# Kernel optimization log

Hardware: AMD Instinct MI355X
Metric: run time of the kernel (lower is better)

Reference implementation:

```python
import jax, jax.numpy as jnp
import numpy as np

T, E, K = 3, 6, 3            # n_tasks, num_experts, top-k
D, H, EH, TH = 1024, 1024, 1024, 1024  # input, hidden, expert hidden, tower hidden
B, C = 1024, 16              # batch, n_candidates


def setup_inputs() -> dict:
    key = jax.random.key(0)
    ks = jax.random.split(key, 16)
    s = 0.02
    return {
        "cls_embed": jax.random.normal(ks[0], (B, C, D), jnp.float32),
        "fc1_w": jax.random.normal(ks[1], (D, H), jnp.float32) * s,
        "fc1_b": jnp.zeros((H,), jnp.float32),
        "fc2_w": jax.random.normal(ks[2], (H, H), jnp.float32) * s,
        "fc2_b": jnp.zeros((H,), jnp.float32),
        "w_gate": jax.random.normal(ks[3], (T, H, E), jnp.float32) * s,
        "ew1": jax.random.normal(ks[4], (E, H, EH), jnp.float32) * s,
        "eb1": jnp.zeros((E, EH), jnp.float32),
        "ew2": jax.random.normal(ks[5], (E, EH, H), jnp.float32) * s,
        "eb2": jnp.zeros((E, H), jnp.float32),
        "tw1": jax.random.normal(ks[6], (T, H, TH), jnp.float32) * s,
        "tb1": jnp.zeros((T, TH), jnp.float32),
        "tw2": jax.random.normal(ks[7], (T, TH), jnp.float32) * s,
        "tb2": jnp.zeros((T,), jnp.float32),
    }


def reference(cls_embed, fc1_w, fc1_b, fc2_w, fc2_b, w_gate,
              ew1, eb1, ew2, eb2, tw1, tb1, tw2, tb2):
    # flatten (batch, candidate) -> N
    x = cls_embed.reshape(-1, cls_embed.shape[-1])            # [N, D]
    # shared bottom: fc2(relu(fc1(x)))
    h = jax.nn.relu(x @ fc1_w + fc1_b) @ fc2_w + fc2_b        # [N, H]
    # per-task top-k gating (clean/eval path of noisy top-k)
    logits = jnp.einsum('nh,the->tne', h, w_gate)             # [T, N, E]
    top_v, top_i = jax.lax.top_k(logits, K)                   # [T, N, K]
    top_w = jax.nn.softmax(top_v, axis=-1)                    # softmax over selected k
    onehot = jax.nn.one_hot(top_i, E, dtype=h.dtype)          # [T, N, K, E]
    gates = jnp.einsum('tnk,tnke->tne', top_w, onehot)        # sparse gate weights
    # experts: two-layer MLPs, computed densely then combined by sparse gates
    eh = jax.nn.relu(jnp.einsum('nh,ehm->nem', h, ew1) + eb1)  # [N, E, EH]
    eo = jnp.einsum('nem,emh->neh', eh, ew2) + eb2             # [N, E, H]
    mo = jnp.einsum('tne,neh->tnh', gates, eo)                 # [T, N, H]
    # per-task towers -> scalar logit per candidate
    th = jax.nn.relu(jnp.einsum('tnh,thm->tnm', mo, tw1) + tb1[:, None, :])
    out = jnp.einsum('tnm,tm->tn', th, tw2) + tb2[:, None]     # [T, N]
    return out
```

## Files before the change

kernel.cpp:

```cpp
#include <hip/hip_runtime.h>
#include <hip/hip_bf16.h>
#include <math.h>
#include <stdint.h>

#define NTOK 16384
#define DH   1024
#define NE   6
#define NT   3

typedef _Float16 f16x8 __attribute__((ext_vector_type(8)));
typedef float    f32x4 __attribute__((ext_vector_type(4)));

__device__ __forceinline__ void stage16(const _Float16* g, _Float16* lds_base, int lane)
{
#if __has_builtin(__builtin_amdgcn_global_load_lds)
    __builtin_amdgcn_global_load_lds(
        (const __attribute__((address_space(1))) unsigned int*)(uintptr_t)g,
        (__attribute__((address_space(3))) unsigned int*)(uintptr_t)lds_base, 16, 0, 0);
#else
    *(float4*)(lds_base + lane * 8) = *(const float4*)g;
#endif
}

__device__ __forceinline__ f32x4 mfma16(f16x8 a, f16x8 b, f32x4 c)
{
    return __builtin_amdgcn_mfma_f32_16x16x32_f16(a, b, c, 0, 0, 0);
}

__device__ __forceinline__ void mfma_tile(const _Float16* __restrict__ A,
                                          const _Float16* __restrict__ Bt,
                                          int n0, int m0, f32x4 acc[4][4])
{
    __shared__ __align__(16) _Float16 As[128 * 32];
    __shared__ __align__(16) _Float16 Bs[128 * 32];
    const int tid  = threadIdx.x;
    const int w    = tid >> 6, lane = tid & 63;
    const int lr   = lane >> 2;
    const int lk   = (lane & 3) * 8;
    const int wm   = (w >> 1) * 64, wn = (w & 1) * 64;
    const int fl   = lane & 15;
    const int fq   = (lane >> 4) * 8;

    const _Float16* ga0 = A  + (size_t)(n0 + w * 32 + lr) * DH + lk;
    const _Float16* ga1 = ga0 + 16 * DH;
    const _Float16* gb0 = Bt + (size_t)(m0 + w * 32 + lr) * DH + lk;
    const _Float16* gb1 = gb0 + 16 * DH;
    _Float16* la0 = As + (w * 32) * 32;
    _Float16* la1 = la0 + 16 * 32;
    _Float16* lb0 = Bs + (w * 32) * 32;
    _Float16* lb1 = lb0 + 16 * 32;

    for (int ks = 0; ks < DH; ks += 32) {
        __syncthreads();
        stage16(ga0 + ks, la0, lane);
        stage16(ga1 + ks, la1, lane);
        stage16(gb0 + ks, lb0, lane);
        stage16(gb1 + ks, lb1, lane);
        __syncthreads();
        f16x8 af[4], bf[4];
#pragma unroll
        for (int i = 0; i < 4; ++i)
            af[i] = *(const f16x8*)(As + (wm + i * 16 + fl) * 32 + fq);
#pragma unroll
        for (int j = 0; j < 4; ++j)
            bf[j] = *(const f16x8*)(Bs + (wn + j * 16 + fl) * 32 + fq);
#pragma unroll
        for (int i = 0; i < 4; ++i)
#pragma unroll
            for (int j = 0; j < 4; ++j)
                acc[i][j] = mfma16(af[i], bf[j], acc[i][j]);
    }
}

__device__ __forceinline__ void mfma_tile_split(const _Float16* __restrict__ Ah,
                                                const _Float16* __restrict__ Al,
                                                const _Float16* __restrict__ Bh,
                                                const _Float16* __restrict__ Bl,
                                                int n0, int m0, f32x4 acc[4][4])
{
    __shared__ __align__(16) _Float16 Ash[128 * 32];
    __shared__ __align__(16) _Float16 Asl[128 * 32];
    __shared__ __align__(16) _Float16 Bsh[128 * 32];
    __shared__ __align__(16) _Float16 Bsl[128 * 32];
    const int tid  = threadIdx.x;
    const int w    = tid >> 6, lane = tid & 63;
    const int lr   = lane >> 2;
    const int lk   = (lane & 3) * 8;
    const int wm   = (w >> 1) * 64, wn = (w & 1) * 64;
    const int fl   = lane & 15;
    const int fq   = (lane >> 4) * 8;

    const size_t ro = (size_t)(n0 + w * 32 + lr) * DH + lk;
    const size_t co = (size_t)(m0 + w * 32 + lr) * DH + lk;
    const int lo0 = (w * 32) * 32, lo1 = lo0 + 16 * 32;

    for (int ks = 0; ks < DH; ks += 32) {
        __syncthreads();
        stage16(Ah + ro + ks,            Ash + lo0, lane);
        stage16(Ah + ro + 16 * DH + ks,  Ash + lo1, lane);
        stage16(Al + ro + ks,            Asl + lo0, lane);
        stage16(Al + ro + 16 * DH + ks,  Asl + lo1, lane);
        stage16(Bh + co + ks,            Bsh + lo0, lane);
        stage16(Bh + co + 16 * DH + ks,  Bsh + lo1, lane);
        stage16(Bl + co + ks,            Bsl + lo0, lane);
        stage16(Bl + co + 16 * DH + ks,  Bsl + lo1, lane);
        __syncthreads();
        f16x8 ah[4], al[4], bh[4], bl[4];
#pragma unroll
        for (int i = 0; i < 4; ++i) {
            const int off = (wm + i * 16 + fl) * 32 + fq;
            ah[i] = *(const f16x8*)(Ash + off);
            al[i] = *(const f16x8*)(Asl + off);
        }
#pragma unroll
        for (int j = 0; j < 4; ++j) {
            const int off = (wn + j * 16 + fl) * 32 + fq;
            bh[j] = *(const f16x8*)(Bsh + off);
            bl[j] = *(const f16x8*)(Bsl + off);
        }
#pragma unroll
        for (int i = 0; i < 4; ++i)
#pragma unroll
            for (int j = 0; j < 4; ++j) {
                acc[i][j] = mfma16(al[i], bh[j], acc[i][j]);
                acc[i][j] = mfma16(ah[i], bl[j], acc[i][j]);
                acc[i][j] = mfma16(ah[i], bh[j], acc[i][j]);
            }
    }
}


__global__ __launch_bounds__(256) void k_fc1(const _Float16* __restrict__ xh,
                                             const _Float16* __restrict__ xl,
                                             const _Float16* __restrict__ wh,
                                             const _Float16* __restrict__ wl,
                                             const float* __restrict__ bias,
                                             _Float16* __restrict__ oh,
                                             _Float16* __restrict__ ol)
{
    f32x4 acc[4][4] = {};
    const int n0 = blockIdx.x * 128, m0 = blockIdx.y * 128;
    mfma_tile_split(xh, xl, wh, wl, n0, m0, acc);
    const int lane = threadIdx.x & 63, w = threadIdx.x >> 6;
    const int wm = (w >> 1) * 64, wn = (w & 1) * 64;
    const int fl = lane & 15, quad = lane >> 4;
#pragma unroll
    for (int i = 0; i < 4; ++i)
#pragma unroll
        for (int reg = 0; reg < 4; ++reg) {
            const int r = n0 + wm + i * 16 + quad * 4 + reg;
#pragma unroll
            for (int j = 0; j < 4; ++j) {
                const int c = m0 + wn + j * 16 + fl;
                const float v = fmaxf(acc[i][j][reg] + bias[c], 0.0f);
                const _Float16 h = (_Float16)v;
                oh[(size_t)r * DH + c] = h;
                ol[(size_t)r * DH + c] = (_Float16)(v - (float)h);
            }
        }
}

__global__ __launch_bounds__(256) void k_fc2(const _Float16* __restrict__ ah,
                                             const _Float16* __restrict__ al,
                                             const _Float16* __restrict__ wh,
                                             const _Float16* __restrict__ wl,
                                             const float* __restrict__ bias,
                                             float* __restrict__ h32,
                                             _Float16* __restrict__ h16)
{
    f32x4 acc[4][4] = {};
    const int n0 = blockIdx.x * 128, m0 = blockIdx.y * 128;
    mfma_tile_split(ah, al, wh, wl, n0, m0, acc);
    const int lane = threadIdx.x & 63, w = threadIdx.x >> 6;
    const int wm = (w >> 1) * 64, wn = (w & 1) * 64;
    const int fl = lane & 15, quad = lane >> 4;
#pragma unroll
    for (int i = 0; i < 4; ++i)
#pragma unroll
        for (int reg = 0; reg < 4; ++reg) {
            const int r = n0 + wm + i * 16 + quad * 4 + reg;
#pragma unroll
            for (int j = 0; j < 4; ++j) {
                const int c = m0 + wn + j * 16 + fl;
                const float v = acc[i][j][reg] + bias[c];
                h32[(size_t)r * DH + c] = v;
                h16[(size_t)r * DH + c] = (_Float16)v;
            }
        }
}

__global__ __launch_bounds__(256) void k_expert1(const _Float16* __restrict__ A,
                                                 const _Float16* __restrict__ ew1t,
                                                 const float* __restrict__ eb1,
                                                 _Float16* __restrict__ eh,
                                                 int chunk)
{
    const int e = blockIdx.z;
    const _Float16* Bt = ew1t + (size_t)e * DH * DH;
    const float* bias  = eb1 + e * DH;
    _Float16* C        = eh + (size_t)e * chunk * DH;

    f32x4 acc[4][4] = {};
    const int n0 = blockIdx.x * 128, m0 = blockIdx.y * 128;
    mfma_tile(A, Bt, n0, m0, acc);
    const int lane = threadIdx.x & 63, w = threadIdx.x >> 6;
    const int wm = (w >> 1) * 64, wn = (w & 1) * 64;
    const int fl = lane & 15, quad = lane >> 4;
#pragma unroll
    for (int i = 0; i < 4; ++i)
#pragma unroll
        for (int reg = 0; reg < 4; ++reg) {
            const int r = n0 + wm + i * 16 + quad * 4 + reg;
#pragma unroll
            for (int j = 0; j < 4; ++j) {
                const int c = m0 + wn + j * 16 + fl;
                C[(size_t)r * DH + c] = (_Float16)fmaxf(acc[i][j][reg] + bias[c], 0.0f);
            }
        }
}

__global__ __launch_bounds__(256) void k_expert2(const _Float16* __restrict__ eh,
                                                 const _Float16* __restrict__ ew2t,
                                                 const float* __restrict__ eb2,
                                                 _Float16* __restrict__ eo,
                                                 int chunk)
{
    const int e = blockIdx.z;
    const _Float16* A  = eh + (size_t)e * chunk * DH;
    const _Float16* Bt = ew2t + (size_t)e * DH * DH;
    const float* bias  = eb2 + e * DH;
    _Float16* C        = eo + (size_t)e * chunk * DH;

    f32x4 acc[4][4] = {};
    const int n0 = blockIdx.x * 128, m0 = blockIdx.y * 128;
    mfma_tile(A, Bt, n0, m0, acc);
    const int lane = threadIdx.x & 63, w = threadIdx.x >> 6;
    const int wm = (w >> 1) * 64, wn = (w & 1) * 64;
    const int fl = lane & 15, quad = lane >> 4;
#pragma unroll
    for (int i = 0; i < 4; ++i)
#pragma unroll
        for (int reg = 0; reg < 4; ++reg) {
            const int r = n0 + wm + i * 16 + quad * 4 + reg;
#pragma unroll
            for (int j = 0; j < 4; ++j) {
                const int c = m0 + wn + j * 16 + fl;
                C[(size_t)r * DH + c] = (_Float16)(acc[i][j][reg] + bias[c]);
            }
        }
}

__global__ __launch_bounds__(256) void k_combine(const _Float16* __restrict__ eo,
                                                 const float* __restrict__ gates,
                                                 _Float16* __restrict__ mo,
                                                 int chunk)
{
    const size_t plane = (size_t)chunk * DH;
    const size_t idx = (size_t)blockIdx.x * 256 + threadIdx.x;
    const size_t off = idx * 8;
    if (off >= plane) return;
    const int n = (int)(off / DH);

    float acc[NT][8] = {};
#pragma unroll
    for (int e = 0; e < NE; ++e) {
        const f16x8 v = *(const f16x8*)(eo + e * plane + off);
        float vf[8];
#pragma unroll
        for (int j = 0; j < 8; ++j) vf[j] = (float)v[j];
#pragma unroll
        for (int t = 0; t < NT; ++t) {
            const float g = gates[(size_t)(e * NT + t) * chunk + n];
#pragma unroll
            for (int j = 0; j < 8; ++j) acc[t][j] += g * vf[j];
        }
    }
#pragma unroll
    for (int t = 0; t < NT; ++t) {
        f16x8 r;
#pragma unroll
        for (int j = 0; j < 8; ++j) r[j] = (_Float16)acc[t][j];
        *(f16x8*)(mo + t * plane + off) = r;
    }
}

__global__ __launch_bounds__(256) void k_mfma_tower(const _Float16* __restrict__ mo,
                                                    const _Float16* __restrict__ tw1t,
                                                    const float* __restrict__ tb1,
                                                    const float* __restrict__ tw2,
                                                    float* __restrict__ out,
                                                    int n_base, int chunk)
{
    const int t = blockIdx.z;
    const _Float16* A  = mo   + (size_t)t * chunk * DH;
    const _Float16* Bt = tw1t + (size_t)t * DH * DH;
    const float* b1 = tb1 + t * DH;
    const float* w2 = tw2 + t * DH;

    f32x4 acc[4][4] = {};
    const int n0 = blockIdx.x * 128, m0 = blockIdx.y * 128;
    mfma_tile(A, Bt, n0, m0, acc);
    const int lane = threadIdx.x & 63, w = threadIdx.x >> 6;
    const int wm = (w >> 1) * 64, wn = (w & 1) * 64;
    const int fl = lane & 15, quad = lane >> 4;

    float s[4][4];
#pragma unroll
    for (int i = 0; i < 4; ++i)
#pragma unroll
        for (int reg = 0; reg < 4; ++reg) {
            float v = 0.0f;
#pragma unroll
            for (int j = 0; j < 4; ++j) {
                const int c = m0 + wn + j * 16 + fl;
                v += fmaxf(acc[i][j][reg] + b1[c], 0.0f) * w2[c];
            }
            s[i][reg] = v;
        }
#pragma unroll
    for (int d = 8; d > 0; d >>= 1)
#pragma unroll
        for (int i = 0; i < 4; ++i)
#pragma unroll
            for (int reg = 0; reg < 4; ++reg)
                s[i][reg] += __shfl_down(s[i][reg], d, 16);
    if (fl == 0) {
#pragma unroll
        for (int i = 0; i < 4; ++i)
#pragma unroll
            for (int reg = 0; reg < 4; ++reg) {
                const int r = n0 + wm + i * 16 + quad * 4 + reg;
                atomicAdd(out + (size_t)t * NTOK + n_base + r, s[i][reg]);
            }
    }
}

__global__ __launch_bounds__(256) void k_gating2(const float* __restrict__ h,
                                                 const double* __restrict__ wgt,
                                                 float* __restrict__ gates,
                                                 int chunk)
{
    const int w = threadIdx.x >> 6, lane = threadIdx.x & 63;
    const int n = blockIdx.x * 4 + w;

    double acc[NT][NE] = {};
#pragma unroll 4
    for (int i = 0; i < 16; ++i) {
        const int k = lane + 64 * i;
        const double hv = (double)h[(size_t)n * DH + k];
#pragma unroll
        for (int t = 0; t < NT; ++t)
#pragma unroll
            for (int e = 0; e < NE; ++e)
                acc[t][e] += hv * wgt[(size_t)(t * NE + e) * DH + k];
    }
#pragma unroll
    for (int d = 1; d < 64; d <<= 1)
#pragma unroll
        for (int t = 0; t < NT; ++t)
#pragma unroll
            for (int e = 0; e < NE; ++e)
                acc[t][e] += __shfl_xor(acc[t][e], d, 64);

    if (lane < NT) {
        const int t = lane;
        double a[NE];
#pragma unroll
        for (int e = 0; e < NE; ++e) a[e] = acc[t][e];
        bool used[NE] = {false, false, false, false, false, false};
        int idx[3];
        double tv[3];
#pragma unroll
        for (int k = 0; k < 3; ++k) {
            int best = -1;
#pragma unroll
            for (int e = 0; e < NE; ++e)
                if (!used[e] && (best < 0 || a[e] > a[best])) best = e;
            used[best] = true;
            idx[k] = best;
            tv[k] = a[best];
        }
        const double m  = tv[0];
        const double w0 = exp(tv[0] - m), w1 = exp(tv[1] - m), w2 = exp(tv[2] - m);
        const double sum = w0 + w1 + w2;
        float g[NE] = {0.f, 0.f, 0.f, 0.f, 0.f, 0.f};
        g[idx[0]] = (float)(w0 / sum);
        g[idx[1]] = (float)(w1 / sum);
        g[idx[2]] = (float)(w2 / sum);
#pragma unroll
        for (int e = 0; e < NE; ++e)
            gates[(size_t)(e * NT + t) * chunk + n] = g[e];
    }
}

__global__ __launch_bounds__(256) void k_init_out(float* __restrict__ out,
                                                  const float* __restrict__ tb2)
{
    const int i = blockIdx.x * 256 + threadIdx.x;
    if (i < NT * NTOK) out[i] = tb2[i >> 14];
}

__global__ __launch_bounds__(256) void k_xsplit(const float* __restrict__ s,
                                                _Float16* __restrict__ hi,
                                                _Float16* __restrict__ lo, int n)
{
    const int i = blockIdx.x * 256 + threadIdx.x;
    if (i < n) {
        const float v = s[i];
        const _Float16 h = (_Float16)v;
        hi[i] = h;
        lo[i] = (_Float16)(v - (float)h);
    }
}

__global__ __launch_bounds__(256) void k_w16t(const float* __restrict__ src,
                                              _Float16* __restrict__ dst)
{
    __shared__ float t[32][33];
    const float* s = src + (size_t)blockIdx.z * DH * DH;
    _Float16* d    = dst + (size_t)blockIdx.z * DH * DH;
    const int k0 = blockIdx.x * 32, m0 = blockIdx.y * 32;
    const int tx = threadIdx.x & 31, ty = threadIdx.x >> 5;
    for (int r = ty; r < 32; r += 8)
        t[r][tx] = s[(size_t)(k0 + r) * DH + m0 + tx];
    __syncthreads();
    for (int r = ty; r < 32; r += 8)
        d[(size_t)(m0 + r) * DH + k0 + tx] = (_Float16)t[tx][r];
}

__global__ __launch_bounds__(256) void k_wsplit_t(const float* __restrict__ src,
                                                  _Float16* __restrict__ dhi,
                                                  _Float16* __restrict__ dlo)
{
    __shared__ float t[32][33];
    const int k0 = blockIdx.x * 32, m0 = blockIdx.y * 32;
    const int tx = threadIdx.x & 31, ty = threadIdx.x >> 5;
    for (int r = ty; r < 32; r += 8)
        t[r][tx] = src[(size_t)(k0 + r) * DH + m0 + tx];
    __syncthreads();
    for (int r = ty; r < 32; r += 8) {
        const float v = t[tx][r];
        const _Float16 h = (_Float16)v;
        dhi[(size_t)(m0 + r) * DH + k0 + tx] = h;
        dlo[(size_t)(m0 + r) * DH + k0 + tx] = (_Float16)(v - (float)h);
    }
}

__global__ __launch_bounds__(256) void k_wg_t(const float* __restrict__ wg,
                                              double* __restrict__ wgt)
{
    const int i = blockIdx.x * 256 + threadIdx.x;
    if (i < NT * NE * DH) {
        const int k = i & (DH - 1);
        const int te = i >> 10;
        const int e = te % NE, t = te / NE;
        wgt[i] = (double)wg[((size_t)t * DH + k) * NE + e];
    }
}

extern "C" void kernel_launch(void* const* d_in, const int* in_sizes, int n_in,
                              void* d_out, int out_size, void* d_ws, size_t ws_size,
                              hipStream_t stream)
{
    const float* x      = (const float*)d_in[0];
    const float* fc1_w  = (const float*)d_in[1];
    const float* fc1_b  = (const float*)d_in[2];
    const float* fc2_w  = (const float*)d_in[3];
    const float* fc2_b  = (const float*)d_in[4];
    const float* w_gate = (const float*)d_in[5];
    const float* ew1    = (const float*)d_in[6];
    const float* eb1    = (const float*)d_in[7];
    const float* ew2    = (const float*)d_in[8];
    const float* eb2    = (const float*)d_in[9];
    const float* tw1    = (const float*)d_in[10];
    const float* tb1    = (const float*)d_in[11];
    const float* tw2    = (const float*)d_in[12];
    const float* tb2    = (const float*)d_in[13];
    float* out = (float*)d_out;

    const size_t plane = (size_t)DH * DH * 2;
    const size_t fixed = 19 * plane + (size_t)NT * NE * DH * 8;
    const size_t per_tok = (size_t)13 * DH * 2 + NE * NT * 4;
    int chunk = 16384;
    while (chunk > 128 && fixed + (size_t)chunk * per_tok > ws_size) chunk >>= 1;

    char* p = (char*)d_ws;
    _Float16* ew1t = (_Float16*)p; p += NE * plane;
    _Float16* ew2t = (_Float16*)p; p += NE * plane;
    _Float16* tw1t = (_Float16*)p; p += NT * plane;
    _Float16* w1th = (_Float16*)p; p += plane;
    _Float16* w1tl = (_Float16*)p; p += plane;
    _Float16* w2th = (_Float16*)p; p += plane;
    _Float16* w2tl = (_Float16*)p; p += plane;
    double* wgt    = (double*)p;   p += (size_t)NT * NE * DH * 8;

    const size_t cpe = (size_t)chunk * DH;
    _Float16* eh   = (_Float16*)p; p += 6 * cpe * 2;
    _Float16* h16  = (_Float16*)p; p += cpe * 2;
    _Float16* eo   = (_Float16*)p; p += 6 * cpe * 2;
    float* gates   = (float*)p;    p += (size_t)NE * NT * chunk * 4;

    _Float16* xh  = eh + 0 * cpe;
    _Float16* xl  = eh + 1 * cpe;
    _Float16* h1h = eh + 2 * cpe;
    _Float16* h1l = eh + 3 * cpe;
    float*    h32 = (float*)(eh + 4 * cpe);
    _Float16* mo  = eh;

    const dim3 blk(256);
    const dim3 gm(chunk / 128, DH / 128);
    const dim3 gme(chunk / 128, DH / 128, NE);

    k_init_out<<<dim3((NT * NTOK + 255) / 256), blk, 0, stream>>>(out, tb2);

    k_w16t<<<dim3(32, 32, NE), blk, 0, stream>>>(ew1, ew1t);
    k_w16t<<<dim3(32, 32, NE), blk, 0, stream>>>(ew2, ew2t);
    k_w16t<<<dim3(32, 32, NT), blk, 0, stream>>>(tw1, tw1t);
    k_wsplit_t<<<dim3(32, 32), blk, 0, stream>>>(fc1_w, w1th, w1tl);
    k_wsplit_t<<<dim3(32, 32), blk, 0, stream>>>(fc2_w, w2th, w2tl);
    k_wg_t<<<dim3((NT * NE * DH + 255) / 256), blk, 0, stream>>>(w_gate, wgt);

    for (int nb = 0; nb < NTOK; nb += chunk) {
        const float* xc = x + (size_t)nb * DH;
        const int nel = (int)cpe;

        k_xsplit<<<dim3((nel + 255) / 256), blk, 0, stream>>>(xc, xh, xl, nel);
        k_fc1<<<gm, blk, 0, stream>>>(xh, xl, w1th, w1tl, fc1_b, h1h, h1l);
        k_fc2<<<gm, blk, 0, stream>>>(h1h, h1l, w2th, w2tl, fc2_b, h32, h16);

        k_gating2<<<dim3(chunk / 4), blk, 0, stream>>>(h32, wgt, gates, chunk);

        k_expert1<<<gme, blk, 0, stream>>>(h16, ew1t, eb1, eh, chunk);
        k_expert2<<<gme, blk, 0, stream>>>(eh, ew2t, eb2, eo, chunk);

        k_combine<<<dim3((unsigned)((cpe / 8 + 255) / 256)), blk, 0, stream>>>(
            eo, gates, mo, chunk);

        k_mfma_tower<<<dim3(chunk / 128, DH / 128, NT), blk, 0, stream>>>(
            mo, tw1t, tb1, tw2, out, nb, chunk);
    }
}
```

Baseline: 1.467 ms.

## Compute gating logits with split-fp16 MFMA and fall back to fp64 only near ties

Gating logits were computed per token in fp64 over all 1024 hidden values. They now come from a three-term hi/lo fp16 MFMA GEMM. A select kernel takes the top-k, builds the gates, and flags tokens whose 3rd and 4th logits are within a small tolerance. Only those flagged tokens rerun the exact fp64 gating, which is meant to skip most of the expensive double-precision work. The x split kernel is also vectorised to 8 elements per thread. In exchange, fc2 writes an extra low-part fp16 buffer, and ties just above the tolerance could pick different experts than exact fp64 would.

Result: slower. 1.607 ms (+9.6%).

```diff
diff --git a/kernel.cpp b/kernel.cpp
--- a/kernel.cpp
+++ b/kernel.cpp
@@ -7,6 +7,7 @@
 #define DH   1024
 #define NE   6
 #define NT   3
+#define TAU  1e-4f
 
 typedef _Float16 f16x8 __attribute__((ext_vector_type(8)));
 typedef float    f32x4 __attribute__((ext_vector_type(4)));
@@ -166,7 +167,8 @@
                                              const _Float16* __restrict__ wl,
                                              const float* __restrict__ bias,
                                              float* __restrict__ h32,
-                                             _Float16* __restrict__ h16)
+                                             _Float16* __restrict__ h16,
+                                             _Float16* __restrict__ h16l)
 {
     f32x4 acc[4][4] = {};
     const int n0 = blockIdx.x * 128, m0 = blockIdx.y * 128;
@@ -183,165 +185,143 @@
             for (int j = 0; j < 4; ++j) {
                 const int c = m0 + wn + j * 16 + fl;
                 const float v = acc[i][j][reg] + bias[c];
+                const _Float16 h = (_Float16)v;
                 h32[(size_t)r * DH + c] = v;
-                h16[(size_t)r * DH + c] = (_Float16)v;
-            }
-        }
-}
-
-__global__ __launch_bounds__(256) void k_expert1(const _Float16* __restrict__ A,
-                                                 const _Float16* __restrict__ ew1t,
-                                                 const float* __restrict__ eb1,
-                                                 _Float16* __restrict__ eh,
-                                                 int chunk)
-{
-    const int e = blockIdx.z;
-    const _Float16* Bt = ew1t + (size_t)e * DH * DH;
-    const float* bias  = eb1 + e * DH;
-    _Float16* C        = eh + (size_t)e * chunk * DH;
-
-    f32x4 acc[4][4] = {};
-    const int n0 = blockIdx.x * 128, m0 = blockIdx.y * 128;
-    mfma_tile(A, Bt, n0, m0, acc);
-    const int lane = threadIdx.x & 63, w = threadIdx.x >> 6;
-    const int wm = (w >> 1) * 64, wn = (w & 1) * 64;
-    const int fl = lane & 15, quad = lane >> 4;
-#pragma unroll
-    for (int i = 0; i < 4; ++i)
+                h16[(size_t)r * DH + c] = h;
+                h16l[(size_t)r * DH + c] = (_Float16)(v - (float)h);
+            }
+        }
+}
+
+__global__ __launch_bounds__(128) void k_logits(const _Float16* __restrict__ hh,
+                                                const _Float16* __restrict__ hl,
+                                                const _Float16* __restrict__ wgh,
+                                                const _Float16* __restrict__ wgl,
+                                                float* __restrict__ logits,
+                                                int chunk)
+{
+    __shared__ __align__(16) _Float16 Ash[64 * 32];
+    __shared__ __align__(16) _Float16 Asl[64 * 32];
+    __shared__ __align__(16) _Float16 Bsh[32 * 32];
+    __shared__ __align__(16) _Float16 Bsl[32 * 32];
+    const int tid = threadIdx.x;
+    const int w = tid >> 6, lane = tid & 63;
+    const int lr = lane >> 2, lk = (lane & 3) * 8;
+    const int fl = lane & 15, fq = (lane >> 4) * 8;
+    const int n0 = blockIdx.x * 64;
+
+    const size_t ro = (size_t)(n0 + w * 32 + lr) * DH + lk;
+    const size_t bo = (size_t)lr * DH + lk;
+    const int la0 = (w * 32) * 32, la1 = la0 + 16 * 32;
+
+    f32x4 acc[2][2] = {};
+    for (int ks = 0; ks < DH; ks += 32) {
+        __syncthreads();
+        stage16(hh + ro + ks,           Ash + la0, lane);
+        stage16(hh + ro + 16 * DH + ks, Ash + la1, lane);
+        stage16(hl + ro + ks,           Asl + la0, lane);
+        stage16(hl + ro + 16 * DH + ks, Asl + la1, lane);
+        if (w == 0) {
+            stage16(wgh + bo + ks,           Bsh,           lane);
+            stage16(wgh + bo + 16 * DH + ks, Bsh + 16 * 32, lane);
+        } else {
+            stage16(wgl + bo + ks,           Bsl,           lane);
+            stage16(wgl + bo + 16 * DH + ks, Bsl + 16 * 32, lane);
+        }
+        __syncthreads();
+        f16x8 ah[2], al[2], bh[2], bl[2];
+#pragma unroll
+        for (int i = 0; i < 2; ++i) {
+            const int off = (w * 32 + i * 16 + fl) * 32 + fq;
+            ah[i] = *(const f16x8*)(Ash + off);
+            al[i] = *(const f16x8*)(Asl + off);
+        }
+#pragma unroll
+        for (int j = 0; j < 2; ++j) {
+            const int off = (j * 16 + fl) * 32 + fq;
+            bh[j] = *(const f16x8*)(Bsh + off);
+            bl[j] = *(const f16x8*)(Bsl + off);
+        }
+#pragma unroll
+        for (int i = 0; i < 2; ++i)
+#pragma unroll
+            for (int j = 0; j < 2; ++j) {
+                acc[i][j] = mfma16(al[i], bh[j], acc[i][j]);
+                acc[i][j] = mfma16(ah[i], bl[j], acc[i][j]);
+                acc[i][j] = mfma16(ah[i], bh[j], acc[i][j]);
+            }
+    }
+    const int quad = lane >> 4;
+#pragma unroll
+    for (int i = 0; i < 2; ++i)
 #pragma unroll
         for (int reg = 0; reg < 4; ++reg) {
-            const int r = n0 + wm + i * 16 + quad * 4 + reg;
-#pragma unroll
-            for (int j = 0; j < 4; ++j) {
-                const int c = m0 + wn + j * 16 + fl;
-                C[(size_t)r * DH + c] = (_Float16)fmaxf(acc[i][j][reg] + bias[c], 0.0f);
-            }
-        }
-}
-
-__global__ __launch_bounds__(256) void k_expert2(const _Float16* __restrict__ eh,
-                                                 const _Float16* __restrict__ ew2t,
-                                                 const float* __restrict__ eb2,
-                                                 _Float16* __restrict__ eo,
-                                                 int chunk)
-{
-    const int e = blockIdx.z;
-    const _Float16* A  = eh + (size_t)e * chunk * DH;
-    const _Float16* Bt = ew2t + (size_t)e * DH * DH;
-    const float* bias  = eb2 + e * DH;
-    _Float16* C        = eo + (size_t)e * chunk * DH;
-
-    f32x4 acc[4][4] = {};
-    const int n0 = blockIdx.x * 128, m0 = blockIdx.y * 128;
-    mfma_tile(A, Bt, n0, m0, acc);
-    const int lane = threadIdx.x & 63, w = threadIdx.x >> 6;
-    const int wm = (w >> 1) * 64, wn = (w & 1) * 64;
-    const int fl = lane & 15, quad = lane >> 4;
-#pragma unroll
-    for (int i = 0; i < 4; ++i)
-#pragma unroll
-        for (int reg = 0; reg < 4; ++reg) {
-            const int r = n0 + wm + i * 16 + quad * 4 + reg;
-#pragma unroll
-            for (int j = 0; j < 4; ++j) {
-                const int c = m0 + wn + j * 16 + fl;
-                C[(size_t)r * DH + c] = (_Float16)(acc[i][j][reg] + bias[c]);
-            }
-        }
-}
-
-__global__ __launch_bounds__(256) void k_combine(const _Float16* __restrict__ eo,
-                                                 const float* __restrict__ gates,
-                                                 _Float16* __restrict__ mo,
-                                                 int chunk)
-{
-    const size_t plane = (size_t)chunk * DH;
-    const size_t idx = (size_t)blockIdx.x * 256 + threadIdx.x;
-    const size_t off = idx * 8;
-    if (off >= plane) return;
-    const int n = (int)(off / DH);
-
-    float acc[NT][8] = {};
-#pragma unroll
-    for (int e = 0; e < NE; ++e) {
-        const f16x8 v = *(const f16x8*)(eo + e * plane + off);
-        float vf[8];
-#pragma unroll
-        for (int j = 0; j < 8; ++j) vf[j] = (float)v[j];
-#pragma unroll
-        for (int t = 0; t < NT; ++t) {
-            const float g = gates[(size_t)(e * NT + t) * chunk + n];
-#pragma unroll
-            for (int j = 0; j < 8; ++j) acc[t][j] += g * vf[j];
-        }
-    }
+            const int r = n0 + w * 32 + i * 16 + quad * 4 + reg;
+#pragma unroll
+            for (int j = 0; j < 2; ++j) {
+                const int c = j * 16 + fl;
+                logits[(size_t)c * chunk + r] = acc[i][j][reg];
+            }
+        }
+}
+
+__global__ __launch_bounds__(256) void k_select(const float* __restrict__ logits,
+                                                float* __restrict__ gates,
+                                                unsigned char* __restrict__ flags,
+                                                int chunk)
+{
+    const int n = blockIdx.x * 256 + threadIdx.x;
+    if (n >= chunk) return;
+    float l[18];
+#pragma unroll
+    for (int c = 0; c < 18; ++c) l[c] = logits[(size_t)c * chunk + n];
+    unsigned char f = 0;
 #pragma unroll
     for (int t = 0; t < NT; ++t) {
-        f16x8 r;
-#pragma unroll
-        for (int j = 0; j < 8; ++j) r[j] = (_Float16)acc[t][j];
-        *(f16x8*)(mo + t * plane + off) = r;
-    }
-}
-
-__global__ __launch_bounds__(256) void k_mfma_tower(const _Float16* __restrict__ mo,
-                                                    const _Float16* __restrict__ tw1t,
-                                                    const float* __restrict__ tb1,
-                                                    const float* __restrict__ tw2,
-                                                    float* __restrict__ out,
-                                                    int n_base, int chunk)
-{
-    const int t = blockIdx.z;
-    const _Float16* A  = mo   + (size_t)t * chunk * DH;
-    const _Float16* Bt = tw1t + (size_t)t * DH * DH;
-    const float* b1 = tb1 + t * DH;
-    const float* w2 = tw2 + t * DH;
-
-    f32x4 acc[4][4] = {};
-    const int n0 = blockIdx.x * 128, m0 = blockIdx.y * 128;
-    mfma_tile(A, Bt, n0, m0, acc);
-    const int lane = threadIdx.x & 63, w = threadIdx.x >> 6;
-    const int wm = (w >> 1) * 64, wn = (w & 1) * 64;
-    const int fl = lane & 15, quad = lane >> 4;
-
-    float s[4][4];
-#pragma unroll
-    for (int i = 0; i < 4; ++i)
-#pragma unroll
-        for (int reg = 0; reg < 4; ++reg) {
-            float v = 0.0f;
-#pragma unroll
-            for (int j = 0; j < 4; ++j) {
-                const int c = m0 + wn + j * 16 + fl;
-                v += fmaxf(acc[i][j][reg] + b1[c], 0.0f) * w2[c];
-            }
-            s[i][reg] = v;
-        }
-#pragma unroll
-    for (int d = 8; d > 0; d >>= 1)
-#pragma unroll
-        for (int i = 0; i < 4; ++i)
-#pragma unroll
-            for (int reg = 0; reg < 4; ++reg)
-                s[i][reg] += __shfl_down(s[i][reg], d, 16);
-    if (fl == 0) {
-#pragma unroll
-        for (int i = 0; i < 4; ++i)
-#pragma unroll
-            for (int reg = 0; reg < 4; ++reg) {
-                const int r = n0 + wm + i * 16 + quad * 4 + reg;
-                atomicAdd(out + (size_t)t * NTOK + n_base + r, s[i][reg]);
-            }
-    }
-}
-
-__global__ __launch_bounds__(256) void k_gating2(const float* __restrict__ h,
-                                                 const double* __restrict__ wgt,
-                                                 float* __restrict__ gates,
-                                                 int chunk)
+        float a[NE];
+#pragma unroll
+        for (int e = 0; e < NE; ++e) a[e] = l[t * NE + e];
+        bool used[NE] = {false, false, false, false, false, false};
+        int idx[3];
+        float tv[3];
+#pragma unroll
+        for (int k = 0; k < 3; ++k) {
+            int best = -1;
+#pragma unroll
+            for (int e = 0; e < NE; ++e)
+                if (!used[e] && (best < 0 || a[e] > a[best])) best = e;
+            used[best] = true;
+            idx[k] = best;
+            tv[k] = a[best];
+        }
+        float v4 = -3.4e38f;
+#pragma unroll
+        for (int e = 0; e < NE; ++e)
+            if (!used[e] && a[e] > v4) v4 = a[e];
+        if (tv[2] - v4 < TAU) f = 1;
+        const float m = tv[0];
+        const float w0 = expf(tv[0] - m), w1 = expf(tv[1] - m), w2 = expf(tv[2] - m);
+        const float s = w0 + w1 + w2;
+        float g[NE] = {0.f, 0.f, 0.f, 0.f, 0.f, 0.f};
+        g[idx[0]] = w0 / s;
+        g[idx[1]] = w1 / s;
+        g[idx[2]] = w2 / s;
+#pragma unroll
+        for (int e = 0; e < NE; ++e)
+            gates[(size_t)(e * NT + t) * chunk + n] = g[e];
+    }
+    flags[n] = f;
+}
+
+__global__ __launch_bounds__(256) void k_rescue(const float* __restrict__ h,
+                                                const double* __restrict__ wgt,
+                                                const unsigned char* __restrict__ flags,
+                                                float* __restrict__ gates,
+                                                int chunk)
 {
     const int w = threadIdx.x >> 6, lane = threadIdx.x & 63;
     const int n = blockIdx.x * 4 + w;
+    if (!flags[n]) return;
 
     double acc[NT][NE] = {};
 #pragma unroll 4
@@ -393,6 +373,152 @@
     }
 }
 
+__global__ __launch_bounds__(256) void k_expert1(const _Float16* __restrict__ A,
+                                                 const _Float16* __restrict__ ew1t,
+                                                 const float* __restrict__ eb1,
+                                                 _Float16* __restrict__ eh,
+                                                 int chunk)
+{
+    const int e = blockIdx.z;
+    const _Float16* Bt = ew1t + (size_t)e * DH * DH;
+    const float* bias  = eb1 + e * DH;
+    _Float16* C        = eh + (size_t)e * chunk * DH;
+
+    f32x4 acc[4][4] = {};
+    const int n0 = blockIdx.x * 128, m0 = blockIdx.y * 128;
+    mfma_tile(A, Bt, n0, m0, acc);
+    const int lane = threadIdx.x & 63, w = threadIdx.x >> 6;
+    const int wm = (w >> 1) * 64, wn = (w & 1) * 64;
+    const int fl = lane & 15, quad = lane >> 4;
+#pragma unroll
+    for (int i = 0; i < 4; ++i)
+#pragma unroll
+        for (int reg = 0; reg < 4; ++reg) {
+            const int r = n0 + wm + i * 16 + quad * 4 + reg;
+#pragma unroll
+            for (int j = 0; j < 4; ++j) {
+                const int c = m0 + wn + j * 16 + fl;
+                C[(size_t)r * DH + c] = (_Float16)fmaxf(acc[i][j][reg] + bias[c], 0.0f);
+            }
+        }
+}
+
+__global__ __launch_bounds__(256) void k_expert2(const _Float16* __restrict__ eh,
+                                                 const _Float16* __restrict__ ew2t,
+                                                 const float* __restrict__ eb2,
+                                                 _Float16* __restrict__ eo,
+                                                 int chunk)
+{
+    const int e = blockIdx.z;
+    const _Float16* A  = eh + (size_t)e * chunk * DH;
+    const _Float16* Bt = ew2t + (size_t)e * DH * DH;
+    const float* bias  = eb2 + e * DH;
+    _Float16* C        = eo + (size_t)e * chunk * DH;
+
+    f32x4 acc[4][4] = {};
+    const int n0 = blockIdx.x * 128, m0 = blockIdx.y * 128;
+    mfma_tile(A, Bt, n0, m0, acc);
+    const int lane = threadIdx.x & 63, w = threadIdx.x >> 6;
+    const int wm = (w >> 1) * 64, wn = (w & 1) * 64;
+    const int fl = lane & 15, quad = lane >> 4;
+#pragma unroll
+    for (int i = 0; i < 4; ++i)
+#pragma unroll
+        for (int reg = 0; reg < 4; ++reg) {
+            const int r = n0 + wm + i * 16 + quad * 4 + reg;
+#pragma unroll
+            for (int j = 0; j < 4; ++j) {
+                const int c = m0 + wn + j * 16 + fl;
+                C[(size_t)r * DH + c] = (_Float16)(acc[i][j][reg] + bias[c]);
+            }
+        }
+}
+
+__global__ __launch_bounds__(256) void k_combine(const _Float16* __restrict__ eo,
+                                                 const float* __restrict__ gates,
+                                                 _Float16* __restrict__ mo,
+                                                 int chunk)
+{
+    const size_t plane = (size_t)chunk * DH;
+    const size_t idx = (size_t)blockIdx.x * 256 + threadIdx.x;
+    const size_t off = idx * 8;
+    if (off >= plane) return;
+    const int n = (int)(off / DH);
+
+    float acc[NT][8] = {};
+#pragma unroll
+    for (int e = 0; e < NE; ++e) {
+        const f16x8 v = *(const f16x8*)(eo + e * plane + off);
+        float vf[8];
+#pragma unroll
+        for (int j = 0; j < 8; ++j) vf[j] = (float)v[j];
+#pragma unroll
+        for (int t = 0; t < NT; ++t) {
+            const float g = gates[(size_t)(e * NT + t) * chunk + n];
+#pragma unroll
+            for (int j = 0; j < 8; ++j) acc[t][j] += g * vf[j];
+        }
+    }
+#pragma unroll
+    for (int t = 0; t < NT; ++t) {
+        f16x8 r;
+#pragma unroll
+        for (int j = 0; j < 8; ++j) r[j] = (_Float16)acc[t][j];
+        *(f16x8*)(mo + t * plane + off) = r;
+    }
+}
+
+__global__ __launch_bounds__(256) void k_mfma_tower(const _Float16* __restrict__ mo,
+                                                    const _Float16* __restrict__ tw1t,
+                                                    const float* __restrict__ tb1,
+                                                    const float* __restrict__ tw2,
+                                                    float* __restrict__ out,
+                                                    int n_base, int chunk)
+{
+    const int t = blockIdx.z;
+    const _Float16* A  = mo   + (size_t)t * chunk * DH;
+    const _Float16* Bt = tw1t + (size_t)t * DH * DH;
+    const float* b1 = tb1 + t * DH;
+    const float* w2 = tw2 + t * DH;
+
+    f32x4 acc[4][4] = {};
+    const int n0 = blockIdx.x * 128, m0 = blockIdx.y * 128;
+    mfma_tile(A, Bt, n0, m0, acc);
+    const int lane = threadIdx.x & 63, w = threadIdx.x >> 6;
+    const int wm = (w >> 1) * 64, wn = (w & 1) * 64;
+    const int fl = lane & 15, quad = lane >> 4;
+
+    float s[4][4];
+#pragma unroll
+    for (int i = 0; i < 4; ++i)
+#pragma unroll
+        for (int reg = 0; reg < 4; ++reg) {
+            float v = 0.0f;
+#pragma unroll
+            for (int j = 0; j < 4; ++j) {
+                const int c = m0 + wn + j * 16 + fl;
+                v += fmaxf(acc[i][j][reg] + b1[c], 0.0f) * w2[c];
+            }
+            s[i][reg] = v;
+        }
+#pragma unroll
+    for (int d = 8; d > 0; d >>= 1)
+#pragma unroll
+        for (int i = 0; i < 4; ++i)
+#pragma unroll
+            for (int reg = 0; reg < 4; ++reg)
+                s[i][reg] += __shfl_down(s[i][reg], d, 16);
+    if (fl == 0) {
+#pragma unroll
+        for (int i = 0; i < 4; ++i)
+#pragma unroll
+            for (int reg = 0; reg < 4; ++reg) {
+                const int r = n0 + wm + i * 16 + quad * 4 + reg;
+                atomicAdd(out + (size_t)t * NTOK + n_base + r, s[i][reg]);
+            }
+    }
+}
+
 __global__ __launch_bounds__(256) void k_init_out(float* __restrict__ out,
                                                   const float* __restrict__ tb2)
 {
@@ -400,17 +526,25 @@
     if (i < NT * NTOK) out[i] = tb2[i >> 14];
 }
 
-__global__ __launch_bounds__(256) void k_xsplit(const float* __restrict__ s,
-                                                _Float16* __restrict__ hi,
-                                                _Float16* __restrict__ lo, int n)
-{
-    const int i = blockIdx.x * 256 + threadIdx.x;
-    if (i < n) {
-        const float v = s[i];
-        const _Float16 h = (_Float16)v;
-        hi[i] = h;
-        lo[i] = (_Float16)(v - (float)h);
-    }
+__global__ __launch_bounds__(256) void k_xsplit8(const float* __restrict__ s,
+                                                 _Float16* __restrict__ hi,
+                                                 _Float16* __restrict__ lo, size_t n8)
+{
+    const size_t i = (size_t)blockIdx.x * 256 + threadIdx.x;
+    if (i >= n8) return;
+    const size_t off = i * 8;
+    const float4 a = *(const float4*)(s + off);
+    const float4 b = *(const float4*)(s + off + 4);
+    const float v[8] = {a.x, a.y, a.z, a.w, b.x, b.y, b.z, b.w};
+    f16x8 H, L;
+#pragma unroll
+    for (int j = 0; j < 8; ++j) {
+        const _Float16 h = (_Float16)v[j];
+        H[j] = h;
+        L[j] = (_Float16)(v[j] - (float)h);
+    }
+    *(f16x8*)(hi + off) = H;
+    *(f16x8*)(lo + off) = L;
 }
 
 __global__ __launch_bounds__(256) void k_w16t(const float* __restrict__ src,
@@ -456,6 +590,24 @@
         const int e = te % NE, t = te / NE;
         wgt[i] = (double)wg[((size_t)t * DH + k) * NE + e];
     }
+}
+
+__global__ __launch_bounds__(256) void k_wgsplit(const float* __restrict__ wg,
+                                                 _Float16* __restrict__ wgh,
+                                                 _Float16* __restrict__ wgl)
+{
+    const int i = blockIdx.x * 256 + threadIdx.x;
+    if (i >= 32 * DH) return;
+    const int k = i & (DH - 1);
+    const int c = i >> 10;
+    float v = 0.0f;
+    if (c < NT * NE) {
+        const int t = c / NE, e = c - t * NE;
+        v = wg[((size_t)t * DH + k) * NE + e];
+    }
+    const _Float16 h = (_Float16)v;
+    wgh[i] = h;
+    wgl[i] = (_Float16)(v - (float)h);
 }
 
 extern "C" void kernel_launch(void* const* d_in, const int* in_sizes, int n_in,
@@ -479,8 +631,8 @@
     float* out = (float*)d_out;
 
     const size_t plane = (size_t)DH * DH * 2;
-    const size_t fixed = 19 * plane + (size_t)NT * NE * DH * 8;
-    const size_t per_tok = (size_t)13 * DH * 2 + NE * NT * 4;
+    const size_t fixed = 19 * plane + (size_t)NT * NE * DH * 8 + (size_t)2 * 32 * DH * 2;
+    const size_t per_tok = (size_t)14 * DH * 2 + NE * NT * 4 + 1;
     int chunk = 16384;
     while (chunk > 128 && fixed + (size_t)chunk * per_tok > ws_size) chunk >>= 1;
 
@@ -493,12 +645,16 @@
     _Float16* w2th = (_Float16*)p; p += plane;
     _Float16* w2tl = (_Float16*)p; p += plane;
     double* wgt    = (double*)p;   p += (size_t)NT * NE * DH * 8;
+    _Float16* wgh  = (_Float16*)p; p += (size_t)32 * DH * 2;
+    _Float16* wgl  = (_Float16*)p; p += (size_t)32 * DH * 2;
 
     const size_t cpe = (size_t)chunk * DH;
     _Float16* eh   = (_Float16*)p; p += 6 * cpe * 2;
     _Float16* h16  = (_Float16*)p; p += cpe * 2;
+    _Float16* h16l = (_Float16*)p; p += cpe * 2;
     _Float16* eo   = (_Float16*)p; p += 6 * cpe * 2;
     float* gates   = (float*)p;    p += (size_t)NE * NT * chunk * 4;
+    unsigned char* flags = (unsigned char*)p; p += chunk;
 
     _Float16* xh  = eh + 0 * cpe;
     _Float16* xl  = eh + 1 * cpe;
@@ -506,6 +662,7 @@
     _Float16* h1l = eh + 3 * cpe;
     float*    h32 = (float*)(eh + 4 * cpe);
     _Float16* mo  = eh;
+    float* logits = (float*)eo;
 
     const dim3 blk(256);
     const dim3 gm(chunk / 128, DH / 128);
@@ -519,16 +676,18 @@
     k_wsplit_t<<<dim3(32, 32), blk, 0, stream>>>(fc1_w, w1th, w1tl);
     k_wsplit_t<<<dim3(32, 32), blk, 0, stream>>>(fc2_w, w2th, w2tl);
     k_wg_t<<<dim3((NT * NE * DH + 255) / 256), blk, 0, stream>>>(w_gate, wgt);
+    k_wgsplit<<<dim3((32 * DH + 255) / 256), blk, 0, stream>>>(w_gate, wgh, wgl);
 
     for (int nb = 0; nb < NTOK; nb += chunk) {
         const float* xc = x + (size_t)nb * DH;
-        const int nel = (int)cpe;
-
-        k_xsplit<<<dim3((nel + 255) / 256), blk, 0, stream>>>(xc, xh, xl, nel);
+
+        k_xsplit8<<<dim3((unsigned)((cpe / 8 + 255) / 256)), blk, 0, stream>>>(xc, xh, xl, cpe / 8);
         k_fc1<<<gm, blk, 0, stream>>>(xh, xl, w1th, w1tl, fc1_b, h1h, h1l);
-        k_fc2<<<gm, blk, 0, stream>>>(h1h, h1l, w2th, w2tl, fc2_b, h32, h16);
-
-        k_gating2<<<dim3(chunk / 4), blk, 0, stream>>>(h32, wgt, gates, chunk);
+        k_fc2<<<gm, blk, 0, stream>>>(h1h, h1l, w2th, w2tl, fc2_b, h32, h16, h16l);
+
+        k_logits<<<dim3(chunk / 64), dim3(128), 0, stream>>>(h16, h16l, wgh, wgl, logits, chunk);
+        k_select<<<dim3(chunk / 256), blk, 0, stream>>>(logits, gates, flags, chunk);
+        k_rescue<<<dim3(chunk / 4), blk, 0, stream>>>(h32, wgt, flags, gates, chunk);
 
         k_expert1<<<gme, blk, 0, stream>>>(h16, ew1t, eb1, eh, chunk);
         k_expert2<<<gme, blk, 0, stream>>>(eh, ew2t, eb2, eo, chunk);
```
